# Performance work log

Hardware: AMD Instinct MI355X
Metric: run time of the kernel (lower is better)

The kernel has to match this reference:

```python
import jax, jax.numpy as jnp
import numpy as np

LN_EPS = 1e-5


def setup_inputs() -> dict:
    key = jax.random.key(0)
    ks = jax.random.split(key, 6)
    B, M, N, D = 16, 128, 128, 128
    NM, H = 16, 512
    xav = float(np.sqrt(2.0 / (D + D)))  # xavier_normal over (in_dim, out_dim) fan
    return {
        "x": jax.random.normal(ks[0], (B, M, N, D), jnp.float32),
        "w1": jax.random.normal(ks[1], (D, D, NM, 2), jnp.float32) * xav,
        "w2": jax.random.normal(ks[2], (D, D, NM, 2), jnp.float32) * xav,
        "ff_w0": jax.random.normal(ks[3], (D, H), jnp.float32) * float(1.0 / np.sqrt(D)),
        "ff_b0": jnp.zeros((H,), jnp.float32),
        "ff_w1": jax.random.normal(ks[4], (H, D), jnp.float32) * float(1.0 / np.sqrt(H)),
        "ff_b1": jnp.zeros((D,), jnp.float32),
        "ln_g": jnp.ones((D,), jnp.float32),
        "ln_b": jnp.zeros((D,), jnp.float32),
    }


def _layer_norm(h, g, b):
    mu = jnp.mean(h, axis=-1, keepdims=True)
    var = jnp.mean(jnp.square(h - mu), axis=-1, keepdims=True)
    return (h - mu) * jax.lax.rsqrt(var + LN_EPS) * g + b


def _forward_fourier(x, w1, w2):
    # x: [B, M, N, I] -> [B, I, M, N]
    xt = jnp.transpose(x, (0, 3, 1, 2))
    B, I, M, N = xt.shape
    nm = w1.shape[2]
    cw1 = w1[..., 0] + 1j * w1[..., 1]  # [I, O, nm]
    cw2 = w2[..., 0] + 1j * w2[..., 1]
    O = cw1.shape[1]

    # Fourier along last axis (y)
    fty = jnp.fft.rfft(xt, axis=-1, norm="ortho")                    # [B,I,M,N//2+1]
    f1 = jnp.einsum("bixy,ioy->boxy", fty[..., :nm], cw1)            # [B,O,M,nm]
    pad_y = jnp.zeros((B, O, M, N // 2 + 1 - nm), dtype=f1.dtype)
    xy = jnp.fft.irfft(jnp.concatenate([f1, pad_y], axis=-1), n=N, axis=-1, norm="ortho")

    # Fourier along second-to-last axis (x)
    ftx = jnp.fft.rfft(xt, axis=-2, norm="ortho")                    # [B,I,M//2+1,N]
    f2 = jnp.einsum("bixy,iox->boxy", ftx[:, :, :nm, :], cw2)        # [B,O,nm,N]
    pad_x = jnp.zeros((B, O, M // 2 + 1 - nm, N), dtype=f2.dtype)
    xx = jnp.fft.irfft(jnp.concatenate([f2, pad_x], axis=-2), n=M, axis=-2, norm="ortho")

    return jnp.transpose(xx + xy, (0, 2, 3, 1))  # [B,M,N,O]


def reference(x, w1, w2, ff_w0, ff_b0, ff_w1, ff_b1, ln_g, ln_b):
    h = _forward_fourier(x, w1, w2)
    # backcast FeedForward: Linear -> ReLU -> Linear -> LayerNorm (dropout=0)
    h1 = jax.nn.relu(jnp.einsum("bmni,ih->bmnh", h, ff_w0) + ff_b0)
    h2 = jnp.einsum("bmnh,ho->bmno", h1, ff_w1) + ff_b1
    return _layer_norm(h2, ln_g, ln_b)
```

## Files before the change

### kernel.cpp

```cpp
#include <hip/hip_runtime.h>


#define LN_EPS 1e-5f
#define NMODES 16
#define FROW 4096
#define HROW 16384

typedef __attribute__((ext_vector_type(8))) short short8;
typedef __attribute__((ext_vector_type(8))) ushort ushort8;
typedef __attribute__((ext_vector_type(4))) short short4v;
typedef __attribute__((ext_vector_type(4))) float f32x4;

__device__ __forceinline__ ushort f2bf(float f) {
    unsigned u = __float_as_uint(f);
    unsigned r = (u + 0x7FFFu + ((u >> 16) & 1u)) >> 16;
    return (ushort)r;
}
__device__ __forceinline__ float bf2f(ushort h) {
    return __uint_as_float(((unsigned)h) << 16);
}

__global__ void k_setup(float* __restrict__ Tc, float* __restrict__ Ts,
                        float* __restrict__ IT) {
    const float invs = 0.08838834764831845f;
    for (int idx = threadIdx.x; idx < NMODES * 128; idx += blockDim.x) {
        int k = idx >> 7, n = idx & 127;
        int p = (k * n) & 127;
        float th = (float)p * (6.283185307179586f / 128.0f);
        float c = cosf(th), s = sinf(th);
        Tc[idx] = c * invs;
        Ts[idx] = -s * invs;
        float ck = (k == 0) ? invs : 2.0f * invs;
        IT[n * 32 + 2 * k]     = ck * c;
        IT[n * 32 + 2 * k + 1] = -ck * s;
    }
}

__global__ void k_wpack(const float* __restrict__ w, ushort* __restrict__ Wph,
                        ushort* __restrict__ Wpl) {
    int idx = blockIdx.x * 256 + threadIdx.x;
    int k  = idx >> 16;
    int op = (idx >> 8) & 255;
    int ip = idx & 255;
    int i = ip & 127, o = op & 127;
    const float* base = w + (((i << 7) | o) * NMODES + k) * 2;
    float re = base[0], im = base[1];
    float v = (ip < 128) ? ((op < 128) ? re : im)
                         : ((op < 128) ? -im : re);
    ushort hi = f2bf(v);
    ushort lo = f2bf(v - bf2f(hi));
    Wph[idx] = hi;
    Wpl[idx] = lo;
}

__global__ __launch_bounds__(256) void k_wcvt(const float* __restrict__ w0,
        const float* __restrict__ w1, ushort* __restrict__ w0t,
        ushort* __restrict__ w1t) {
    int idx = blockIdx.x * 256 + threadIdx.x;
    int h = idx >> 7, k = idx & 127;
    w0t[idx] = f2bf(w0[k * 512 + h]);
    int o = idx >> 9, hh = idx & 511;
    w1t[idx] = f2bf(w1[hh * 128 + o]);
}

__global__ __launch_bounds__(128) void k_fft(const float* __restrict__ x,
        const float* __restrict__ Tc, const float* __restrict__ Ts,
        float* __restrict__ F, int mode) {
    __shared__ float Tc_s[NMODES * 128];
    __shared__ float Ts_s[NMODES * 128];
    for (int e = threadIdx.x; e < NMODES * 128; e += 128) {
        Tc_s[e] = Tc[e];
        Ts_s[e] = Ts[e];
    }
    __syncthreads();
    int row = blockIdx.x;
    int base, ts;
    if (mode == 0) { base = row * HROW; ts = 128; }
    else { base = (row >> 7) * 2097152 + (row & 127) * 128; ts = 16384; }
    int i = threadIdx.x;
    float re[NMODES], im[NMODES];
#pragma unroll
    for (int k = 0; k < NMODES; ++k) { re[k] = 0.f; im[k] = 0.f; }
    for (int tb = 0; tb < 32; ++tb) {
        int t0 = tb * 4;
        float xv0 = x[base + (t0 + 0) * ts + i];
        float xv1 = x[base + (t0 + 1) * ts + i];
        float xv2 = x[base + (t0 + 2) * ts + i];
        float xv3 = x[base + (t0 + 3) * ts + i];
#pragma unroll
        for (int k = 0; k < NMODES; ++k) {
            f32x4 c4 = *(const f32x4*)&Tc_s[k * 128 + t0];
            f32x4 s4 = *(const f32x4*)&Ts_s[k * 128 + t0];
            re[k] += xv0 * c4[0] + xv1 * c4[1] + xv2 * c4[2] + xv3 * c4[3];
            im[k] += xv0 * s4[0] + xv1 * s4[1] + xv2 * s4[2] + xv3 * s4[3];
        }
    }
    float* outp = F + row * FROW;
#pragma unroll
    for (int k = 0; k < NMODES; ++k) {
        outp[k * 256 + i]       = re[k];
        outp[k * 256 + 128 + i] = im[k];
    }
}

__global__ __launch_bounds__(256) void k_mixm(const float* __restrict__ A,
        const ushort* __restrict__ Wph, const ushort* __restrict__ Wpl,
        float* __restrict__ outF) {
    __shared__ ushort Ah[32 * 264];
    __shared__ ushort Al[32 * 264];
    int tid = threadIdx.x;
    int kt = blockIdx.x & 15;
    int bm0 = (blockIdx.x >> 4) * 32;
    {
        int row = tid >> 3, cg = tid & 7;
        const float* arow = A + (bm0 + row) * FROW + kt * 256 + cg * 32;
        ushort* ah = &Ah[row * 264 + cg * 32];
        ushort* al = &Al[row * 264 + cg * 32];
#pragma unroll
        for (int j = 0; j < 8; ++j) {
            f32x4 v = *(const f32x4*)(arow + j * 4);
            short4v h4, l4;
#pragma unroll
            for (int q = 0; q < 4; ++q) {
                ushort h = f2bf(v[q]);
                h4[q] = (short)h;
                l4[q] = (short)f2bf(v[q] - bf2f(h));
            }
            *(short4v*)(ah + j * 4) = h4;
            *(short4v*)(al + j * 4) = l4;
        }
    }
    __syncthreads();
    int lane = tid & 63, wid = tid >> 6;
    int frow = lane & 15, fk8 = (lane >> 4) * 8, fr4 = (lane >> 4) * 4;
    f32x4 acc[2][4];
#pragma unroll
    for (int a = 0; a < 2; ++a)
#pragma unroll
        for (int c = 0; c < 4; ++c) acc[a][c] = {0.f, 0.f, 0.f, 0.f};
    const ushort* wph = Wph + kt * 65536;
    const ushort* wpl = Wpl + kt * 65536;
#pragma unroll
    for (int kk = 0; kk < 8; ++kk) {
        short8 ah0 = *(const short8*)&Ah[(frow)      * 264 + kk * 32 + fk8];
        short8 ah1 = *(const short8*)&Ah[(16 + frow) * 264 + kk * 32 + fk8];
        short8 al0 = *(const short8*)&Al[(frow)      * 264 + kk * 32 + fk8];
        short8 al1 = *(const short8*)&Al[(16 + frow) * 264 + kk * 32 + fk8];
#pragma unroll
        for (int tc = 0; tc < 4; ++tc) {
            int op = wid * 64 + tc * 16 + frow;
            int base = op * 256 + kk * 32 + fk8;
            short8 wh = *(const short8*)&wph[base];
            short8 wl = *(const short8*)&wpl[base];
            acc[0][tc] = __builtin_amdgcn_mfma_f32_16x16x32_bf16(ah0, wh, acc[0][tc], 0, 0, 0);
            acc[0][tc] = __builtin_amdgcn_mfma_f32_16x16x32_bf16(ah0, wl, acc[0][tc], 0, 0, 0);
            acc[0][tc] = __builtin_amdgcn_mfma_f32_16x16x32_bf16(al0, wh, acc[0][tc], 0, 0, 0);
            acc[1][tc] = __builtin_amdgcn_mfma_f32_16x16x32_bf16(ah1, wh, acc[1][tc], 0, 0, 0);
            acc[1][tc] = __builtin_amdgcn_mfma_f32_16x16x32_bf16(ah1, wl, acc[1][tc], 0, 0, 0);
            acc[1][tc] = __builtin_amdgcn_mfma_f32_16x16x32_bf16(al1, wh, acc[1][tc], 0, 0, 0);
        }
    }
#pragma unroll
    for (int tr = 0; tr < 2; ++tr)
#pragma unroll
        for (int tc = 0; tc < 4; ++tc)
#pragma unroll
            for (int r = 0; r < 4; ++r)
                outF[(bm0 + tr * 16 + fr4 + r) * FROW + kt * 256 + wid * 64 + tc * 16 + frow]
                    = acc[tr][tc][r];
}

__global__ __launch_bounds__(256) void k_icdft(const float* __restrict__ f,
        const float* __restrict__ IT, ushort* __restrict__ obf,
        float* __restrict__ h32, ushort* __restrict__ hbfs, int mode) {
    __shared__ float IT_s[128 * 32];
    __shared__ float f_s[32 * 128];
    int row = blockIdx.x;
    for (int e = threadIdx.x; e < 4096; e += 256) {
        IT_s[e] = IT[e];
        f_s[e]  = f[row * FROW + e];
    }
    __syncthreads();
    int o = threadIdx.x & 127, nh = threadIdx.x >> 7;
    for (int nb = 0; nb < 8; ++nb) {
        int n0 = nh * 64 + nb * 8;
        float acc[8];
#pragma unroll
        for (int j = 0; j < 8; ++j) acc[j] = 0.f;
#pragma unroll
        for (int kpb = 0; kpb < 8; ++kpb) {
            int kp0 = kpb * 4;
            float f0 = f_s[kp0 * 128 + o];
            float f1v = f_s[kp0 * 128 + 128 + o];
            float f2v = f_s[kp0 * 128 + 256 + o];
            float f3v = f_s[kp0 * 128 + 384 + o];
#pragma unroll
            for (int j = 0; j < 8; ++j) {
                f32x4 it = *(const f32x4*)&IT_s[(n0 + j) * 32 + kp0];
                acc[j] += f0 * it[0] + f1v * it[1] + f2v * it[2] + f3v * it[3];
            }
        }
        if (mode == 0) {
#pragma unroll
            for (int j = 0; j < 8; ++j)
                obf[row * HROW + (n0 + j) * 128 + o] = f2bf(acc[j]);
        } else if (mode == 1) {
#pragma unroll
            for (int j = 0; j < 8; ++j)
                h32[row * HROW + (n0 + j) * 128 + o] = acc[j];
        } else {
#pragma unroll
            for (int j = 0; j < 8; ++j) {
                int ix = (row >> 7) * 2097152 + (row & 127) * 128 + o + (n0 + j) * 16384;
                hbfs[ix] = f2bf(h32[ix] + acc[j]);
            }
        }
    }
}

__global__ __launch_bounds__(64, 2) void k_ffn(const ushort* __restrict__ hy,
        const ushort* __restrict__ hx, const ushort* __restrict__ hbfs,
        float* __restrict__ out,
        const ushort* __restrict__ w0t, const float* __restrict__ b0,
        const ushort* __restrict__ w1t, const float* __restrict__ b1,
        const float* __restrict__ g, const float* __restrict__ bb, int two) {
    __shared__ __align__(16) ushort h_s[64 * 134];
    __shared__ __align__(16) ushort h1_s[64 * 38];
    int lane = threadIdx.x;
    int R0 = blockIdx.x * 64;

    if (two) {
        int b = R0 >> 14, m = (R0 >> 7) & 127, n0 = R0 & 127;
        const ushort* hyp = hy + (size_t)R0 * 128;
        const ushort* hxp = hx + (size_t)b * 2097152 + (size_t)n0 * 16384 + m * 128;
#pragma unroll
        for (int half = 0; half < 2; ++half) {
            ushort8 ay[8], ax[8];
#pragma unroll
            for (int i = 0; i < 8; ++i) {
                int e = lane + (half * 8 + i) * 64;
                int rl = e >> 4, c8 = (e & 15) * 8;
                ay[i] = *(const ushort8*)&hyp[rl * 128 + c8];
                ax[i] = *(const ushort8*)&hxp[rl * 16384 + c8];
            }
#pragma unroll
            for (int i = 0; i < 8; ++i) {
                int e = lane + (half * 8 + i) * 64;
                int rl = e >> 4, c8 = (e & 15) * 8;
                ushort8 t;
#pragma unroll
                for (int j = 0; j < 8; ++j) t[j] = f2bf(bf2f(ay[i][j]) + bf2f(ax[i][j]));
                *(ushort8*)&h_s[rl * 134 + c8] = t;
            }
        }
    } else {
#pragma unroll
        for (int i = 0; i < 16; ++i) {
            int e = lane + i * 64;
            int rl = e >> 4, c8 = (e & 15) * 8;
            *(ushort8*)&h_s[rl * 134 + c8] =
                *(const ushort8*)&hbfs[(size_t)(R0 + rl) * 128 + c8];
        }
    }
    __syncthreads();

    int frow = lane & 15, qg = lane >> 4;
    int fk8 = qg * 8, fr4 = qg * 4;

    f32x4 acc2[4][8];
#pragma unroll
    for (int a = 0; a < 4; ++a)
#pragma unroll
        for (int c = 0; c < 8; ++c) acc2[a][c] = {0.f, 0.f, 0.f, 0.f};

    short8 bfr[2][4];
#pragma unroll
    for (int tc2 = 0; tc2 < 2; ++tc2)
#pragma unroll
        for (int kk = 0; kk < 4; ++kk)
            bfr[tc2][kk] = *(const short8*)&w0t[(tc2 * 16 + frow) * 128 + kk * 32 + fk8];

#pragma unroll 1
    for (int ch = 0; ch < 16; ++ch) {
        short8 b2[8];
#pragma unroll
        for (int tc = 0; tc < 8; ++tc)
            b2[tc] = *(const short8*)&w1t[(tc * 16 + frow) * 512 + ch * 32 + fk8];
        float b0v0 = b0[ch * 32 + frow];
        float b0v1 = b0[ch * 32 + 16 + frow];

#pragma unroll
        for (int g2 = 0; g2 < 2; ++g2) {
            f32x4 acc1[2][2];
#pragma unroll
            for (int a = 0; a < 2; ++a)
#pragma unroll
                for (int c = 0; c < 2; ++c) acc1[a][c] = {0.f, 0.f, 0.f, 0.f};
#pragma unroll
            for (int kk = 0; kk < 4; ++kk)
#pragma unroll
                for (int t2 = 0; t2 < 2; ++t2) {
                    int tr = g2 * 2 + t2;
                    short8 av = *(const short8*)&h_s[(tr * 16 + frow) * 134 + kk * 32 + fk8];
                    acc1[t2][0] = __builtin_amdgcn_mfma_f32_16x16x32_bf16(
                        av, bfr[0][kk], acc1[t2][0], 0, 0, 0);
                    acc1[t2][1] = __builtin_amdgcn_mfma_f32_16x16x32_bf16(
                        av, bfr[1][kk], acc1[t2][1], 0, 0, 0);
                }
#pragma unroll
            for (int t2 = 0; t2 < 2; ++t2)
#pragma unroll
                for (int r = 0; r < 4; ++r) {
                    int rowl = (g2 * 2 + t2) * 16 + fr4 + r;
                    h1_s[rowl * 38 + frow] =
                        f2bf(fmaxf(acc1[t2][0][r] + b0v0, 0.f));
                    h1_s[rowl * 38 + 16 + frow] =
                        f2bf(fmaxf(acc1[t2][1][r] + b0v1, 0.f));
                }
        }

        if (ch < 15) {
#pragma unroll
            for (int tc2 = 0; tc2 < 2; ++tc2)
#pragma unroll
                for (int kk = 0; kk < 4; ++kk)
                    bfr[tc2][kk] = *(const short8*)
                        &w0t[((ch + 1) * 32 + tc2 * 16 + frow) * 128 + kk * 32 + fk8];
        }

#pragma unroll
        for (int tr = 0; tr < 4; ++tr) {
            short8 a2 = *(const short8*)&h1_s[(tr * 16 + frow) * 38 + fk8];
#pragma unroll
            for (int tc = 0; tc < 8; ++tc)
                acc2[tr][tc] = __builtin_amdgcn_mfma_f32_16x16x32_bf16(
                    a2, b2[tc], acc2[tr][tc], 0, 0, 0);
        }
    }

    float b1v[8], gv[8], bv[8];
#pragma unroll
    for (int tc = 0; tc < 8; ++tc) {
        int o = tc * 16 + frow;
        b1v[tc] = b1[o]; gv[tc] = g[o]; bv[tc] = bb[o];
    }
#pragma unroll
    for (int tr = 0; tr < 4; ++tr)
#pragma unroll
        for (int r = 0; r < 4; ++r) {
            float s = 0.f, qq = 0.f;
#pragma unroll
            for (int tc = 0; tc < 8; ++tc) {
                float v = acc2[tr][tc][r] + b1v[tc];
                acc2[tr][tc][r] = v;
                s += v; qq += v * v;
            }
            s += __shfl_xor(s, 1); qq += __shfl_xor(qq, 1);
            s += __shfl_xor(s, 2); qq += __shfl_xor(qq, 2);
            s += __shfl_xor(s, 4); qq += __shfl_xor(qq, 4);
            s += __shfl_xor(s, 8); qq += __shfl_xor(qq, 8);
            float mu = s * (1.0f / 128.0f);
            float var = qq * (1.0f / 128.0f) - mu * mu;
            float rs = rsqrtf(fmaxf(var, 0.f) + LN_EPS);
            float* orow = &out[(size_t)(R0 + tr * 16 + fr4 + r) * 128];
#pragma unroll
            for (int tc = 0; tc < 8; ++tc)
                orow[tc * 16 + frow] = (acc2[tr][tc][r] - mu) * rs * gv[tc] + bv[tc];
        }
}

extern "C" void kernel_launch(void* const* d_in, const int* in_sizes, int n_in,
                              void* d_out, int out_size, void* d_ws, size_t ws_size,
                              hipStream_t stream) {
    (void)in_sizes; (void)n_in; (void)out_size;
    const float* x   = (const float*)d_in[0];
    const float* w1  = (const float*)d_in[1];
    const float* w2  = (const float*)d_in[2];
    const float* fw0 = (const float*)d_in[3];
    const float* fb0 = (const float*)d_in[4];
    const float* fw1 = (const float*)d_in[5];
    const float* fb1 = (const float*)d_in[6];
    const float* lng = (const float*)d_in[7];
    const float* lnb = (const float*)d_in[8];
    float* out = (float*)d_out;

    char* ws = (char*)d_ws;
    float*  Tc  = (float*)(ws);
    float*  Ts  = (float*)(ws + 8192);
    float*  IT  = (float*)(ws + 16384);
    ushort* Wph = (ushort*)(ws + 32768);
    ushort* Wpl = (ushort*)(ws + 32768 + 2097152);
    ushort* w0t = (ushort*)(ws + 4227072);
    ushort* w1t = (ushort*)(ws + 4358144);
    float*  buf0 = (float*)(ws + 4489216);
    ushort* hy   = (ushort*)(ws + 38043648);
    ushort* hx   = (ushort*)(ws + 105152512);
    const size_t need_two = 172261376ull;
    int two = (ws_size >= need_two) ? 1 : 0;
    ushort* hbfs = hy;

    k_setup<<<1, 256, 0, stream>>>(Tc, Ts, IT);
    k_wcvt <<<256, 256, 0, stream>>>(fw0, fw1, w0t, w1t);

    k_wpack<<<4096, 256, 0, stream>>>(w1, Wph, Wpl);
    k_fft  <<<2048, 128, 0, stream>>>(x, Tc, Ts, buf0, 0);
    k_mixm <<<1024, 256, 0, stream>>>(buf0, Wph, Wpl, buf0);
    if (two) k_icdft<<<2048, 256, 0, stream>>>(buf0, IT, hy, out, hbfs, 0);
    else     k_icdft<<<2048, 256, 0, stream>>>(buf0, IT, hy, out, hbfs, 1);

    k_wpack<<<4096, 256, 0, stream>>>(w2, Wph, Wpl);
    k_fft  <<<2048, 128, 0, stream>>>(x, Tc, Ts, buf0, 1);
    k_mixm <<<1024, 256, 0, stream>>>(buf0, Wph, Wpl, buf0);
    if (two) k_icdft<<<2048, 256, 0, stream>>>(buf0, IT, hx, out, hbfs, 0);
    else     k_icdft<<<2048, 256, 0, stream>>>(buf0, IT, hx, out, hbfs, 2);

    k_ffn<<<4096, 64, 0, stream>>>(hy, hx, hbfs, out, w0t, fb0, w1t, fb1, lng, lnb, two);
}
```

Measured before the change: 604.3 us.

## Fuse hy+hx summation into second icdft and swizzle FFN shared memory

The second inverse-DFT pass now reads the bf16 hy result and writes the summed bf16 hidden state directly, so the FFN kernel loads a single contiguous input instead of gathering hy and a strided hx and adding them. The FFN shared buffers switch from padded layouts to XOR-swizzled layouts meant to avoid LDS bank conflicts without padding. The icdft epilogue now performs strided bf16 reads of hy, which may cost some bandwidth there.

```diff
diff --git a/kernel.cpp b/kernel.cpp
--- a/kernel.cpp
+++ b/kernel.cpp
@@ -172,7 +172,7 @@
 
 __global__ __launch_bounds__(256) void k_icdft(const float* __restrict__ f,
         const float* __restrict__ IT, ushort* __restrict__ obf,
-        float* __restrict__ h32, ushort* __restrict__ hbfs, int mode) {
+        float* __restrict__ h32, const ushort* __restrict__ hyin, int mode) {
     __shared__ float IT_s[128 * 32];
     __shared__ float f_s[32 * 128];
     int row = blockIdx.x;
@@ -208,64 +208,48 @@
 #pragma unroll
             for (int j = 0; j < 8; ++j)
                 h32[row * HROW + (n0 + j) * 128 + o] = acc[j];
-        } else {
+        } else if (mode == 2) {
 #pragma unroll
             for (int j = 0; j < 8; ++j) {
                 int ix = (row >> 7) * 2097152 + (row & 127) * 128 + o + (n0 + j) * 16384;
-                hbfs[ix] = f2bf(h32[ix] + acc[j]);
+                obf[ix] = f2bf(bf2f(hyin[ix]) + acc[j]);
             }
-        }
-    }
-}
-
-__global__ __launch_bounds__(64, 2) void k_ffn(const ushort* __restrict__ hy,
-        const ushort* __restrict__ hx, const ushort* __restrict__ hbfs,
+        } else {
+#pragma unroll
+            for (int j = 0; j < 8; ++j) {
+                int ix = (row >> 7) * 2097152 + (row & 127) * 128 + o + (n0 + j) * 16384;
+                obf[ix] = f2bf(h32[ix] + acc[j]);
+            }
+        }
+    }
+}
+
+__global__ __launch_bounds__(64, 2) void k_ffn(const ushort* __restrict__ hin,
         float* __restrict__ out,
         const ushort* __restrict__ w0t, const float* __restrict__ b0,
         const ushort* __restrict__ w1t, const float* __restrict__ b1,
-        const float* __restrict__ g, const float* __restrict__ bb, int two) {
-    __shared__ __align__(16) ushort h_s[64 * 134];
-    __shared__ __align__(16) ushort h1_s[64 * 38];
+        const float* __restrict__ g, const float* __restrict__ bb) {
+    __shared__ __align__(16) char h_raw[16384];
+    __shared__ __align__(16) char h1_raw[4096];
     int lane = threadIdx.x;
     int R0 = blockIdx.x * 64;
 
-    if (two) {
-        int b = R0 >> 14, m = (R0 >> 7) & 127, n0 = R0 & 127;
-        const ushort* hyp = hy + (size_t)R0 * 128;
-        const ushort* hxp = hx + (size_t)b * 2097152 + (size_t)n0 * 16384 + m * 128;
-#pragma unroll
-        for (int half = 0; half < 2; ++half) {
-            ushort8 ay[8], ax[8];
-#pragma unroll
-            for (int i = 0; i < 8; ++i) {
-                int e = lane + (half * 8 + i) * 64;
-                int rl = e >> 4, c8 = (e & 15) * 8;
-                ay[i] = *(const ushort8*)&hyp[rl * 128 + c8];
-                ax[i] = *(const ushort8*)&hxp[rl * 16384 + c8];
-            }
-#pragma unroll
-            for (int i = 0; i < 8; ++i) {
-                int e = lane + (half * 8 + i) * 64;
-                int rl = e >> 4, c8 = (e & 15) * 8;
-                ushort8 t;
-#pragma unroll
-                for (int j = 0; j < 8; ++j) t[j] = f2bf(bf2f(ay[i][j]) + bf2f(ax[i][j]));
-                *(ushort8*)&h_s[rl * 134 + c8] = t;
-            }
-        }
-    } else {
-#pragma unroll
+    {
+        const ushort* src = hin + (size_t)R0 * 128;
+#pragma unroll 4
         for (int i = 0; i < 16; ++i) {
             int e = lane + i * 64;
-            int rl = e >> 4, c8 = (e & 15) * 8;
-            *(ushort8*)&h_s[rl * 134 + c8] =
-                *(const ushort8*)&hbfs[(size_t)(R0 + rl) * 128 + c8];
+            int rl = e >> 4, c8 = e & 15;
+            ushort8 v = *(const ushort8*)(src + rl * 128 + c8 * 8);
+            *(ushort8*)(h_raw + rl * 256 + ((c8 ^ (rl & 7)) << 4)) = v;
         }
     }
     __syncthreads();
 
     int frow = lane & 15, qg = lane >> 4;
     int fk8 = qg * 8, fr4 = qg * 4;
+    int sw7 = frow & 7;
+    int sw3 = frow & 3;
 
     f32x4 acc2[4][8];
 #pragma unroll
@@ -300,8 +284,9 @@
             for (int kk = 0; kk < 4; ++kk)
 #pragma unroll
                 for (int t2 = 0; t2 < 2; ++t2) {
-                    int tr = g2 * 2 + t2;
-                    short8 av = *(const short8*)&h_s[(tr * 16 + frow) * 134 + kk * 32 + fk8];
+                    int row = (g2 * 2 + t2) * 16 + frow;
+                    short8 av = *(const short8*)(h_raw + row * 256
+                                 + (((kk * 4 + qg) ^ sw7) << 4));
                     acc1[t2][0] = __builtin_amdgcn_mfma_f32_16x16x32_bf16(
                         av, bfr[0][kk], acc1[t2][0], 0, 0, 0);
                     acc1[t2][1] = __builtin_amdgcn_mfma_f32_16x16x32_bf16(
@@ -312,9 +297,9 @@
 #pragma unroll
                 for (int r = 0; r < 4; ++r) {
                     int rowl = (g2 * 2 + t2) * 16 + fr4 + r;
-                    h1_s[rowl * 38 + frow] =
+                    *(ushort*)(h1_raw + rowl * 64 + ((frow * 2) ^ (r << 4))) =
                         f2bf(fmaxf(acc1[t2][0][r] + b0v0, 0.f));
-                    h1_s[rowl * 38 + 16 + frow] =
+                    *(ushort*)(h1_raw + rowl * 64 + (((16 + frow) * 2) ^ (r << 4))) =
                         f2bf(fmaxf(acc1[t2][1][r] + b0v1, 0.f));
                 }
         }
@@ -330,7 +315,8 @@
 
 #pragma unroll
         for (int tr = 0; tr < 4; ++tr) {
-            short8 a2 = *(const short8*)&h1_s[(tr * 16 + frow) * 38 + fk8];
+            int row = tr * 16 + frow;
+            short8 a2 = *(const short8*)(h1_raw + row * 64 + ((qg ^ sw3) << 4));
 #pragma unroll
             for (int tc = 0; tc < 8; ++tc)
                 acc2[tr][tc] = __builtin_amdgcn_mfma_f32_16x16x32_bf16(
@@ -394,7 +380,7 @@
     ushort* w1t = (ushort*)(ws + 4358144);
     float*  buf0 = (float*)(ws + 4489216);
     ushort* hy   = (ushort*)(ws + 38043648);
-    ushort* hx   = (ushort*)(ws + 105152512);
+    ushort* hsum = (ushort*)(ws + 105152512);
     const size_t need_two = 172261376ull;
     int two = (ws_size >= need_two) ? 1 : 0;
     ushort* hbfs = hy;
@@ -405,14 +391,15 @@
     k_wpack<<<4096, 256, 0, stream>>>(w1, Wph, Wpl);
     k_fft  <<<2048, 128, 0, stream>>>(x, Tc, Ts, buf0, 0);
     k_mixm <<<1024, 256, 0, stream>>>(buf0, Wph, Wpl, buf0);
-    if (two) k_icdft<<<2048, 256, 0, stream>>>(buf0, IT, hy, out, hbfs, 0);
-    else     k_icdft<<<2048, 256, 0, stream>>>(buf0, IT, hy, out, hbfs, 1);
+    if (two) k_icdft<<<2048, 256, 0, stream>>>(buf0, IT, hy, out, hy, 0);
+    else     k_icdft<<<2048, 256, 0, stream>>>(buf0, IT, hy, out, hy, 1);
 
     k_wpack<<<4096, 256, 0, stream>>>(w2, Wph, Wpl);
     k_fft  <<<2048, 128, 0, stream>>>(x, Tc, Ts, buf0, 1);
     k_mixm <<<1024, 256, 0, stream>>>(buf0, Wph, Wpl, buf0);
-    if (two) k_icdft<<<2048, 256, 0, stream>>>(buf0, IT, hx, out, hbfs, 0);
-    else     k_icdft<<<2048, 256, 0, stream>>>(buf0, IT, hx, out, hbfs, 2);
-
-    k_ffn<<<4096, 64, 0, stream>>>(hy, hx, hbfs, out, w0t, fb0, w1t, fb1, lng, lnb, two);
-}
+    if (two) k_icdft<<<2048, 256, 0, stream>>>(buf0, IT, hsum, out, hy, 2);
+    else     k_icdft<<<2048, 256, 0, stream>>>(buf0, IT, hbfs, out, hy, 3);
+
+    k_ffn<<<4096, 64, 0, stream>>>(two ? hsum : hbfs, out,
+                                   w0t, fb0, w1t, fb1, lng, lnb);
+}
```

Result: faster. 549.3 us (-9.1%).
